# Optimization experiments

Hardware: AMD Instinct MI355X
Metric: run time of the kernel (lower is better)

## Reference

```python
import jax, jax.numpy as jnp
import numpy as np

B, N, D, L, H, DH, M, FF = 4, 2048, 512, 6, 8, 64, 266, 2048
EPS_LN = 1e-5
KERNEL_EPS = 1e-4


def fixed_pos_emb(n, dim):
    # performer_pytorch FixedPositionalEmbedding: cat(sin, cos) over half-dims
    inv_freq = 1.0 / (10000.0 ** (jnp.arange(0, dim, 2, dtype=jnp.float32) / dim))
    t = jnp.arange(n, dtype=jnp.float32)
    s = jnp.einsum('i,j->ij', t, inv_freq)  # [n, dim//2]
    return jnp.concatenate([jnp.sin(s), jnp.cos(s)], axis=-1)  # [n, dim]


def layer_norm(x, g, b):
    mu = x.mean(-1, keepdims=True)
    var = ((x - mu) ** 2).mean(-1, keepdims=True)
    return (x - mu) * jax.lax.rsqrt(var + EPS_LN) * g + b


def rotate_every_two(t):
    t1 = t[..., ::2]
    t2 = t[..., 1::2]
    return jnp.stack([-t2, t1], axis=-1).reshape(t.shape)


def apply_rotary(q, k, sinu):
    # sinu: [n, DH] = cat(sin_half, cos_half); repeat each value twice (interleaved)
    half = sinu.shape[-1] // 2
    sin = jnp.repeat(sinu[:, :half], 2, axis=-1)  # [n, DH]
    cos = jnp.repeat(sinu[:, half:], 2, axis=-1)
    q = q * cos + rotate_every_two(q) * sin
    k = k * cos + rotate_every_two(k) * sin
    return q, k


def softmax_kernel(data, proj, is_query):
    # data: [B,H,N,DH], proj: [M,DH]
    d = data.shape[-1]
    data_normalizer = d ** -0.25
    ratio = proj.shape[0] ** -0.5
    data_dash = jnp.einsum('bhnd,md->bhnm', data * data_normalizer, proj)
    diag = (data ** 2).sum(-1) * 0.5 * (data_normalizer ** 2)  # [B,H,N]
    if is_query:
        m = jnp.max(data_dash, axis=-1, keepdims=True)
    else:
        m = jnp.max(data_dash)
    return ratio * (jnp.exp(data_dash - diag[..., None] - m) + KERNEL_EPS)


def linear_attention(qf, kf, v):
    # qf/kf: [B,H,N,M], v: [B,H,N,DH]  (non-causal FAVOR+)
    k_sum = kf.sum(axis=-2)  # [B,H,M]
    d_inv = 1.0 / jnp.einsum('bhnm,bhm->bhn', qf, k_sum)
    context = jnp.einsum('bhnm,bhne->bhme', kf, v)  # [B,H,M,DH]
    return jnp.einsum('bhme,bhnm,bhn->bhne', context, qf, d_inv)


def setup_inputs() -> dict:
    key = jax.random.key(0)
    ks = jax.random.split(key, 8)
    std = 0.02
    inp = {
        'x': jax.random.normal(ks[0], (B, N, D), jnp.float32),
        'Wq': jax.random.normal(ks[1], (L, D, H * DH), jnp.float32) * std,
        'Wk': jax.random.normal(ks[2], (L, D, H * DH), jnp.float32) * std,
        'Wv': jax.random.normal(ks[3], (L, D, H * DH), jnp.float32) * std,
        'Wo': jax.random.normal(ks[4], (L, H * DH, D), jnp.float32) * std,
        'proj': jax.random.normal(ks[5], (L, M, DH), jnp.float32),
        'ln1_g': jnp.ones((L, D), jnp.float32),
        'ln1_b': jnp.zeros((L, D), jnp.float32),
        'W1': jax.random.normal(ks[6], (L, D, FF), jnp.float32) * std,
        'b1': jnp.zeros((L, FF), jnp.float32),
        'W2': jax.random.normal(ks[7], (L, FF, D), jnp.float32) * std,
        'b2': jnp.zeros((L, D), jnp.float32),
        'ln2_g': jnp.ones((L, D), jnp.float32),
        'ln2_b': jnp.zeros((L, D), jnp.float32),
        'lnf_g': jnp.ones((D,), jnp.float32),
        'lnf_b': jnp.zeros((D,), jnp.float32),
    }
    return inp


def reference(x, Wq, Wk, Wv, Wo, proj, ln1_g, ln1_b, W1, b1, W2, b2, ln2_g, ln2_b, lnf_g, lnf_b):
    n = x.shape[1]
    x = x + fixed_pos_emb(n, D)[None]          # additive sinusoidal emb
    sinu = fixed_pos_emb(n, DH)                 # per-head rotary table [n, DH]
    for i in range(L):
        # --- PreLayerNorm FAVOR+ self-attention ---
        h = layer_norm(x, ln1_g[i], ln1_b[i])
        q = jnp.einsum('bnd,de->bne', h, Wq[i]).reshape(B, n, H, DH).transpose(0, 2, 1, 3)
        k = jnp.einsum('bnd,de->bne', h, Wk[i]).reshape(B, n, H, DH).transpose(0, 2, 1, 3)
        v = jnp.einsum('bnd,de->bne', h, Wv[i]).reshape(B, n, H, DH).transpose(0, 2, 1, 3)
        q, k = apply_rotary(q, k, sinu)
        qf = softmax_kernel(q, proj[i], True)
        kf = softmax_kernel(k, proj[i], False)
        o = linear_attention(qf, kf, v)         # [B,H,n,DH]
        o = o.transpose(0, 2, 1, 3).reshape(B, n, H * DH)
        x = x + jnp.einsum('bne,ed->bnd', o, Wo[i])
        # --- PreLayerNorm FFN (GELU) ---
        h = layer_norm(x, ln2_g[i], ln2_b[i])
        h = jax.nn.gelu(jnp.einsum('bnd,df->bnf', h, W1[i]) + b1[i], approximate=False)
        x = x + jnp.einsum('bnf,fd->bnd', h, W2[i]) + b2[i]
    return layer_norm(x, lnf_g, lnf_b)
```

## Files before the change

kernel.cpp:

```cpp
#include <hip/hip_runtime.h>
#include <hip/hip_bf16.h>
#include <cstdint>

typedef float v4f __attribute__((ext_vector_type(4)));
typedef short v8s __attribute__((ext_vector_type(8)));
typedef unsigned short u16;

#define N_SEQ 2048
#define D_MODEL 512
#define N_LAYER 6
#define N_HEAD 8
#define D_HEAD 64
#define M_FEAT 266
#define M_PAD 288
#define M_ALLOC 384
#define FF_DIM 2048
#define BATCH 4
#define ROWS 8192
#define BHN 65536

__device__ __forceinline__ float b2f(u16 u) {
  return __uint_as_float(((uint32_t)u) << 16);
}
__device__ __forceinline__ u16 f2b(float f) {
  union { __hip_bfloat16 h; u16 u; } c;
  c.h = __float2bfloat16(f);
  return c.u;
}
__device__ __forceinline__ float wave_sum(float v) {
#pragma unroll
  for (int o = 1; o < 64; o <<= 1) v += __shfl_xor(v, o);
  return v;
}
__device__ __forceinline__ float wave_max(float v) {
#pragma unroll
  for (int o = 1; o < 64; o <<= 1) v = fmaxf(v, __shfl_xor(v, o));
  return v;
}

__device__ __forceinline__ float gelu_f(float x) {
  float ax = fabsf(x) * 0.70710678118f;
  float tt = __builtin_amdgcn_rcpf(fmaf(0.3275911f, ax, 1.0f));
  float poly = tt * fmaf(tt, fmaf(tt, fmaf(tt, fmaf(tt, 1.061405429f, -1.453152027f),
                                           1.421413741f), -0.284496736f), 0.254829592f);
  float er = 1.0f - poly * __expf(-ax * ax);
  er = copysignf(er, x);
  return 0.5f * x * (1.0f + er);
}

__device__ __forceinline__ void mfma_bf16(v4f& d, v8s a, v8s b) {
  asm volatile("v_mfma_f32_16x16x32_bf16 %0, %1, %2, %0" : "+v"(d) : "v"(a), "v"(b));
}

__device__ __forceinline__ void async16(const u16* g, u16* l) {
  __builtin_amdgcn_global_load_lds(
      (const __attribute__((address_space(1))) uint32_t*)g,
      (__attribute__((address_space(3))) uint32_t*)l, 16, 0, 0);
}

template <int EPI, int KSPLIT>
__global__ void __launch_bounds__(512, 4)
gemm3s(const u16* __restrict__ A, const u16* __restrict__ B,
       void* __restrict__ Cv, const float* __restrict__ bias,
       int K, int ldc)
{
  extern __shared__ u16 lds[];
  const int t = threadIdx.x;
  const int lane = t & 63;
  const int w = t >> 6;
  const int wm = w >> 2;
  const int wn = w & 3;
  const int tiM = blockIdx.x << 7, tiN = blockIdx.y << 8;
  const int ks = (KSPLIT > 1) ? blockIdx.z : 0;
  const int kchunk = K / KSPLIT;
  const int NT = kchunk >> 5;

  const int rr = lane & 15;
  const int kq = (lane >> 4) << 3;
  const int sw = ((rr >> 1) & 3) << 3;
  const int cr = kq ^ sw;

  const int srow = t >> 2;
  const int scol = (((t & 3) ^ ((srow >> 1) & 3)) << 3);
  const u16* Abase = A + (long long)(tiM + srow) * K + scol + (long long)ks * kchunk;
  const u16* Bbase = B + (long long)(tiN + srow) * K + scol + (long long)ks * kchunk;
  const long long r128 = 128LL * K;

  v4f acc[4][4] = {};

  auto stage3 = [&](int s, int kt) {
    const long long k0 = (long long)kt * 32;
    u16* d = &lds[s * 12288 + t * 8];
    async16(Abase + k0, d);
    async16(Bbase + k0, d + 4096);
    async16(Bbase + k0 + r128, d + 8192);
  };

  stage3(0, 0);
  stage3(1, 1);
  asm volatile("s_waitcnt vmcnt(3)" ::: "memory");
  __builtin_amdgcn_s_barrier();

  for (int kt = 0; kt < NT; ++kt) {
    const int s = kt % 3;
    const int sp = (kt + 2) % 3;
    const bool st = (kt + 2 < NT);
    const int ab = s * 12288;
    const int bb = ab + 4096;
    v8s af[4], bf[4];
#pragma unroll
    for (int i = 0; i < 4; i++) {
      af[i] = *(const v8s*)&lds[ab + (wm * 64 + i * 16 + rr) * 32 + cr];
      bf[i] = *(const v8s*)&lds[bb + (wn * 64 + i * 16 + rr) * 32 + cr];
    }
    if (st) stage3(sp, kt + 2);
    __builtin_amdgcn_s_setprio(1);
#pragma unroll
    for (int m = 0; m < 4; m++)
#pragma unroll
      for (int n = 0; n < 4; n++) mfma_bf16(acc[m][n], af[m], bf[n]);
    __builtin_amdgcn_s_setprio(0);
    if (st) asm volatile("s_waitcnt vmcnt(3)" ::: "memory");
    else    asm volatile("s_waitcnt vmcnt(0)" ::: "memory");
    __builtin_amdgcn_s_barrier();
  }

  __builtin_amdgcn_sched_barrier(0);
  asm volatile("s_nop 7\ns_nop 7\ns_nop 7");
  __builtin_amdgcn_sched_barrier(0);

  const int r4 = (lane >> 4) << 2;
  const int cc = lane & 15;
#pragma unroll
  for (int mf = 0; mf < 4; mf++)
#pragma unroll
    for (int nf = 0; nf < 4; nf++)
#pragma unroll
      for (int i = 0; i < 4; i++) {
        int row = tiM + wm * 64 + mf * 16 + r4 + i;
        int col = tiN + wn * 64 + nf * 16 + cc;
        float v = acc[mf][nf][i];
        if (EPI == 0) {
          ((u16*)Cv)[(long long)row * ldc + col] = f2b(v);
        } else if (EPI == 3) {
          ((u16*)Cv)[(long long)row * ldc + col] = f2b(gelu_f(v + bias[col]));
        } else {
          ((float*)Cv)[((long long)ks * ROWS + row) * ldc + col] = v;
        }
      }
}

__global__ void ff2red(const float* __restrict__ part, const float* __restrict__ bias,
                       float* __restrict__ x)
{
  long long i = ((long long)blockIdx.x * 256 + threadIdx.x) * 8;
  int col = (int)(i & 511);
  v4f s0 = {}, s1 = {};
#pragma unroll
  for (int ks = 0; ks < 4; ks++) {
    const float* p = part + (long long)ks * (ROWS * 512LL) + i;
    s0 += *(const v4f*)p;
    s1 += *(const v4f*)(p + 4);
  }
  v4f b0 = *(const v4f*)(bias + col);
  v4f b1 = *(const v4f*)(bias + col + 4);
  v4f x0 = *(const v4f*)(x + i), x1 = *(const v4f*)(x + i + 4);
  x0 += s0 + b0;
  x1 += s1 + b1;
  *(v4f*)(x + i) = x0;
  *(v4f*)(x + i + 4) = x1;
}

template <int EPI, int BN, int KSPLIT>
__global__ void __launch_bounds__(256, 4)
gemm2(const u16* __restrict__ A, const u16* __restrict__ B,
      void* __restrict__ Cv, const float* __restrict__ bias,
      int K, int ldc, long long sA, long long sB, long long sC,
      float scale, int Ncap, int Mcap, unsigned int* __restrict__ gmax)
{
  __shared__ u16 As[2][128 * 32];
  __shared__ u16 Bs[2][BN * 32];
  __shared__ float smax[4];
  const int zz = blockIdx.z;
  const int z = (KSPLIT > 1) ? zz / KSPLIT : zz;
  const int ks = (KSPLIT > 1) ? zz % KSPLIT : 0;
  const int kchunk = K / KSPLIT;
  const u16* Ag = A + (long long)z * sA + ks * kchunk;
  const u16* Bg = B + (long long)z * sB + ks * kchunk;
  const int t = threadIdx.x;
  const int lane = t & 63;
  const int w = t >> 6;
  constexpr int NF = BN / 32;
  const int wm = (w >> 1) << 6;
  const int wn = (w & 1) * (BN / 2);
  const int tiM = blockIdx.x << 7, tiN = blockIdx.y * BN;

  const int srow = t >> 2;
  const int scol = (t & 3) << 3;
  const u16* Ap = Ag + (long long)(tiM + srow) * K + scol;
  const u16* Bp = Bg + (long long)(tiN + srow) * K + scol;
  const long long rstride = 64LL * K;

  const int rr = lane & 15;
  const int kc = (lane >> 4) << 3;

  v4f acc[4][NF] = {};

  const int nk = kchunk >> 5;
  auto stage = [&](int buf, int k0) {
    async16(Ap + k0, &As[buf][t * 8]);
    async16(Ap + k0 + rstride, &As[buf][t * 8 + 2048]);
    async16(Bp + k0, &Bs[buf][t * 8]);
    if (BN == 128) async16(Bp + k0 + rstride, &Bs[buf][t * 8 + 2048]);
  };

  stage(0, 0);
  __syncthreads();
  int cur = 0;
  for (int kt = 0; kt < nk; ++kt) {
    if (kt + 1 < nk) stage(cur ^ 1, (kt + 1) << 5);
    v8s af[4], bf[NF];
#pragma unroll
    for (int i = 0; i < 4; i++) af[i] = *(const v8s*)&As[cur][(wm + rr + i * 16) * 32 + kc];
#pragma unroll
    for (int i = 0; i < NF; i++) bf[i] = *(const v8s*)&Bs[cur][(wn + rr + i * 16) * 32 + kc];
#pragma unroll
    for (int fm = 0; fm < 4; fm++)
#pragma unroll
      for (int fn = 0; fn < NF; fn++)
        mfma_bf16(acc[fm][fn], af[fm], bf[fn]);
    __syncthreads();
    cur ^= 1;
  }

  __builtin_amdgcn_sched_barrier(0);
  asm volatile("s_nop 7\ns_nop 7\ns_nop 7");
  __builtin_amdgcn_sched_barrier(0);

  const int r4 = (lane >> 4) << 2;
  const int cc = lane & 15;
  float lmax = -3e38f;
#pragma unroll
  for (int fm = 0; fm < 4; fm++)
#pragma unroll
    for (int fn = 0; fn < NF; fn++)
#pragma unroll
      for (int i = 0; i < 4; i++) {
        int row = tiM + wm + fm * 16 + r4 + i;
        int col = tiN + wn + fn * 16 + cc;
        float v = acc[fm][fn][i];
        if (EPI == 5) {
          if (row < Mcap && col < Ncap)
            ((float*)Cv)[((long long)zz * M_ALLOC + row) * 64 + col] = v;
        } else if (EPI == 7) {
          if (col < M_FEAT) lmax = fmaxf(lmax, v * scale);
        }
      }

  if (EPI == 7) {
    lmax = wave_max(lmax);
    if (lane == 0) smax[w] = lmax;
    __syncthreads();
    if (t == 0) {
      float m = fmaxf(fmaxf(smax[0], smax[1]), fmaxf(smax[2], smax[3]));
      unsigned int u = __float_as_uint(m);
      unsigned int key = (u & 0x80000000u) ? ~u : (u | 0x80000000u);
      atomicMax(gmax, key);
    }
  }
}

__global__ void __launch_bounds__(384, 3)
kf_gemm(const u16* __restrict__ kr, const u16* __restrict__ proj,
        const float* __restrict__ diagk, const unsigned int* __restrict__ kmax,
        u16* __restrict__ kfT, float* __restrict__ part)
{
  __shared__ u16 As[2][288 * 32];
  __shared__ u16 Bs[2][64 * 32];
  __shared__ float sdg[64];
  const int ntile = blockIdx.x;
  const int bh = blockIdx.z;
  const int n0 = ntile << 6;
  const int t = threadIdx.x;
  const int lane = t & 63;
  const int w = t >> 6;
  const u16* Bg = kr + (long long)bh * (N_SEQ * 64) + (long long)n0 * 64;
  const int rr = lane & 15, kc = (lane >> 4) << 3;

  if (t < 64) sdg[t] = diagk[(long long)bh * N_SEQ + n0 + t];
  unsigned int kk = kmax[0];
  const float km = (kk & 0x80000000u) ? __uint_as_float(kk ^ 0x80000000u)
                                      : __uint_as_float(~kk);

  v4f acc[3][4] = {};
  auto stage = [&](int buf, int k0) {
#pragma unroll
    for (int j = 0; j < 3; j++) {
      int idx = j * 384 + t;
      async16(proj + (long long)(idx >> 2) * 64 + ((idx & 3) << 3) + k0,
              &As[buf][j * 3072 + t * 8]);
    }
    if (t < 256) async16(Bg + (long long)(t >> 2) * 64 + ((t & 3) << 3) + k0,
                         &Bs[buf][t * 8]);
  };

  stage(0, 0);
  __syncthreads();
  for (int kt = 0; kt < 2; ++kt) {
    if (kt == 0) stage(1, 32);
    v8s af[3], bf[4];
#pragma unroll
    for (int i = 0; i < 3; i++) af[i] = *(const v8s*)&As[kt][(w * 48 + i * 16 + rr) * 32 + kc];
#pragma unroll
    for (int i = 0; i < 4; i++) bf[i] = *(const v8s*)&Bs[kt][(i * 16 + rr) * 32 + kc];
#pragma unroll
    for (int fm = 0; fm < 3; fm++)
#pragma unroll
      for (int fn = 0; fn < 4; fn++)
        mfma_bf16(acc[fm][fn], af[fm], bf[fn]);
    __syncthreads();
  }

  __builtin_amdgcn_sched_barrier(0);
  asm volatile("s_nop 7\ns_nop 7\ns_nop 7");
  __builtin_amdgcn_sched_barrier(0);

  const int r4 = (lane >> 4) << 2;
  const int cc = lane & 15;
  const float sc = 0.35355339f;

#pragma unroll
  for (int fm = 0; fm < 3; fm++)
#pragma unroll
    for (int i = 0; i < 4; i++) {
      int m = w * 48 + fm * 16 + r4 + i;
      float s = 0.0f;
#pragma unroll
      for (int fn = 0; fn < 4; fn++) {
        float dd = acc[fm][fn][i] * sc;
        float kf = (m < M_FEAT)
            ? 0.06131389f * (__expf(dd - sdg[fn * 16 + cc] - km) + 1e-4f) : 0.0f;
        acc[fm][fn][i] = kf;
        s += kf;
        kfT[((long long)bh * M_ALLOC + m) * N_SEQ + n0 + fn * 16 + cc] = f2b(kf);
      }
#pragma unroll
      for (int o = 1; o < 16; o <<= 1) s += __shfl_xor(s, o);
      if (cc == 0) part[((long long)bh * M_PAD + m) * 32 + ntile] = s;
    }
}

__global__ void ksumred(const float* __restrict__ part, float* __restrict__ ksum)
{
  int i = blockIdx.x * 256 + threadIdx.x;
  if (i >= 32 * M_PAD) return;
  const float* p = part + (long long)i * 32;
  float s = 0.0f;
#pragma unroll
  for (int j = 0; j < 32; j += 4) {
    v4f v = *(const v4f*)(p + j);
    s += v[0] + v[1] + v[2] + v[3];
  }
  ksum[i] = s;
}

template <int EPI>
__global__ void __launch_bounds__(256, 6)
gemm_small(const u16* __restrict__ A, const u16* __restrict__ B,
           void* __restrict__ Cv, const float* __restrict__ bias,
           int K, int ldc, long long sA, long long sB)
{
  __shared__ u16 As[2][64 * 32];
  __shared__ u16 Bs[2][64 * 32];
  const int z = blockIdx.z;
  const u16* Ag = A + (long long)z * sA;
  const u16* Bg = B + (long long)z * sB;
  const int t = threadIdx.x;
  const int lane = t & 63;
  const int w = t >> 6;
  const int wm = (w >> 1) << 5;
  const int wn = (w & 1) << 5;
  const int tiM = blockIdx.x << 6, tiN = blockIdx.y << 6;

  const int srow = t >> 2;
  const int scol = (t & 3) << 3;
  const u16* Ap = Ag + (long long)(tiM + srow) * K + scol;
  const u16* Bp = Bg + (long long)(tiN + srow) * K + scol;

  const int rr = lane & 15;
  const int kc = (lane >> 4) << 3;

  v4f acc[2][2] = {};

  const int nk = K >> 5;
  auto stage = [&](int buf, int k0) {
    async16(Ap + k0, &As[buf][t * 8]);
    async16(Bp + k0, &Bs[buf][t * 8]);
  };

  stage(0, 0);
  __syncthreads();
  int cur = 0;
  for (int kt = 0; kt < nk; ++kt) {
    if (kt + 1 < nk) stage(cur ^ 1, (kt + 1) << 5);
    v8s af[2], bf[2];
#pragma unroll
    for (int i = 0; i < 2; i++) af[i] = *(const v8s*)&As[cur][(wm + rr + i * 16) * 32 + kc];
#pragma unroll
    for (int i = 0; i < 2; i++) bf[i] = *(const v8s*)&Bs[cur][(wn + rr + i * 16) * 32 + kc];
#pragma unroll
    for (int fm = 0; fm < 2; fm++)
#pragma unroll
      for (int fn = 0; fn < 2; fn++)
        mfma_bf16(acc[fm][fn], af[fm], bf[fn]);
    __syncthreads();
    cur ^= 1;
  }

  __builtin_amdgcn_sched_barrier(0);
  asm volatile("s_nop 7\ns_nop 7\ns_nop 7");
  __builtin_amdgcn_sched_barrier(0);

  const int r4 = (lane >> 4) << 2;
  const int cc = lane & 15;
#pragma unroll
  for (int fm = 0; fm < 2; fm++)
#pragma unroll
    for (int fn = 0; fn < 2; fn++)
#pragma unroll
      for (int i = 0; i < 4; i++) {
        int row = tiM + wm + fm * 16 + r4 + i;
        int col = tiN + wn + fn * 16 + cc;
        float v = acc[fm][fn][i];
        if (EPI == 2) {
          long long idx = (long long)row * ldc + col;
          float bb = bias ? bias[col] : 0.0f;
          ((float*)Cv)[idx] += v + bb;
        } else {
          int b_ = z >> 3, h_ = z & 7;
          ((u16*)Cv)[(long long)(b_ * N_SEQ + row) * 512 + h_ * 64 + col] = f2b(v);
        }
      }
}

__global__ void __launch_bounds__(384, 3)
ddq_qf(const u16* __restrict__ qr, const u16* __restrict__ proj,
       const float* __restrict__ diag, const float* __restrict__ ksum,
       u16* __restrict__ qf)
{
  __shared__ u16 As[2][64 * 32];
  __shared__ u16 Bs[2][288 * 32];
  __shared__ float redw[6][64];
  __shared__ float rowv[64];
  __shared__ float sdg[64];
  const int bh = blockIdx.z;
  const int tiM = blockIdx.x << 6;
  const int t = threadIdx.x;
  const int lane = t & 63;
  const int w = t >> 6;
  const u16* Ag = qr + (long long)bh * (N_SEQ * 64);
  const int srow = t >> 2, scol = (t & 3) << 3;
  const u16* Ap = Ag + (long long)(tiM + srow) * 64 + scol;
  const int rr = lane & 15, kc = (lane >> 4) << 3;
  const int wn = w * 48;

  if (t < 64) sdg[t] = diag[(long long)bh * N_SEQ + tiM + t];

  v4f acc[4][3] = {};
  auto stage = [&](int buf, int k0) {
    if (t < 256) async16(Ap + k0, &As[buf][t * 8]);
#pragma unroll
    for (int j = 0; j < 3; j++) {
      int idx = j * 384 + t;
      async16(proj + (long long)(idx >> 2) * 64 + ((idx & 3) << 3) + k0,
              &Bs[buf][j * 3072 + t * 8]);
    }
  };

  stage(0, 0);
  __syncthreads();
  for (int kt = 0; kt < 2; ++kt) {
    if (kt == 0) stage(1, 32);
    v8s af[4], bf[3];
#pragma unroll
    for (int i = 0; i < 4; i++) af[i] = *(const v8s*)&As[kt][(rr + i * 16) * 32 + kc];
#pragma unroll
    for (int i = 0; i < 3; i++) bf[i] = *(const v8s*)&Bs[kt][(wn + i * 16 + rr) * 32 + kc];
#pragma unroll
    for (int fm = 0; fm < 4; fm++)
#pragma unroll
      for (int fn = 0; fn < 3; fn++)
        mfma_bf16(acc[fm][fn], af[fm], bf[fn]);
    __syncthreads();
  }

  __builtin_amdgcn_sched_barrier(0);
  asm volatile("s_nop 7\ns_nop 7\ns_nop 7");
  __builtin_amdgcn_sched_barrier(0);

  const int r4 = (lane >> 4) << 2;
  const int cc = lane & 15;
  const float sc = 0.35355339f;

#pragma unroll
  for (int fm = 0; fm < 4; fm++)
#pragma unroll
    for (int i = 0; i < 4; i++) {
      float m = -3e38f;
#pragma unroll
      for (int fn = 0; fn < 3; fn++) {
        int col = wn + fn * 16 + cc;
        float v = acc[fm][fn][i] * sc;
        if (col < M_FEAT) m = fmaxf(m, v);
      }
#pragma unroll
      for (int o = 1; o < 16; o <<= 1) m = fmaxf(m, __shfl_xor(m, o));
      if (cc == 0) redw[w][fm * 16 + r4 + i] = m;
    }
  __syncthreads();
  if (t < 64) {
    float g = redw[0][t];
#pragma unroll
    for (int ww = 1; ww < 6; ww++) g = fmaxf(g, redw[ww][t]);
    rowv[t] = g;
  }
  __syncthreads();

  float ksv[3];
#pragma unroll
  for (int fn = 0; fn < 3; fn++) ksv[fn] = ksum[bh * M_PAD + wn + fn * 16 + cc];

#pragma unroll
  for (int fm = 0; fm < 4; fm++)
#pragma unroll
    for (int i = 0; i < 4; i++) {
      int row = fm * 16 + r4 + i;
      float gm = rowv[row];
      float dg = sdg[row];
      float s = 0.0f;
#pragma unroll
      for (int fn = 0; fn < 3; fn++) {
        float e = 0.06131389f * (__expf(acc[fm][fn][i] * sc - dg - gm) + 1e-4f);
        acc[fm][fn][i] = e;
        s += e * ksv[fn];
      }
#pragma unroll
      for (int o = 1; o < 16; o <<= 1) s += __shfl_xor(s, o);
      if (cc == 0) redw[w][row] = s;
    }
  __syncthreads();
  if (t < 64) {
    float s = redw[0][t];
#pragma unroll
    for (int ww = 1; ww < 6; ww++) s += redw[ww][t];
    rowv[t] = 1.0f / s;
  }
  __syncthreads();

#pragma unroll
  for (int fm = 0; fm < 4; fm++)
#pragma unroll
    for (int i = 0; i < 4; i++) {
      int row = fm * 16 + r4 + i;
      float dinv = rowv[row];
#pragma unroll
      for (int fn = 0; fn < 3; fn++) {
        int col = wn + fn * 16 + cc;
        qf[((long long)bh * N_SEQ + tiM + row) * M_PAD + col] =
            f2b(acc[fm][fn][i] * dinv);
      }
    }
}

template <bool F32OUT>
__global__ void ln_kernel(const float* __restrict__ x, const float* __restrict__ g,
                          const float* __restrict__ b, void* __restrict__ out)
{
  const int row = blockIdx.x * 4 + (threadIdx.x >> 6);
  const int lane = threadIdx.x & 63;
  const float* xr = x + (long long)row * D_MODEL + lane * 8;
  v4f v0 = *(const v4f*)xr;
  v4f v1 = *(const v4f*)(xr + 4);
  float s = v0[0] + v0[1] + v0[2] + v0[3] + v1[0] + v1[1] + v1[2] + v1[3];
  float sq = v0[0]*v0[0] + v0[1]*v0[1] + v0[2]*v0[2] + v0[3]*v0[3]
           + v1[0]*v1[0] + v1[1]*v1[1] + v1[2]*v1[2] + v1[3]*v1[3];
  s = wave_sum(s);
  sq = wave_sum(sq);
  float mu = s * (1.0f / D_MODEL);
  float var = sq * (1.0f / D_MODEL) - mu * mu;
  float rstd = rsqrtf(var + 1e-5f);
  v4f g0 = *(const v4f*)(g + lane * 8), g1 = *(const v4f*)(g + lane * 8 + 4);
  v4f bb0 = *(const v4f*)(b + lane * 8), bb1 = *(const v4f*)(b + lane * 8 + 4);
  float y[8];
#pragma unroll
  for (int j = 0; j < 4; j++) y[j] = (v0[j] - mu) * rstd * g0[j] + bb0[j];
#pragma unroll
  for (int j = 0; j < 4; j++) y[4 + j] = (v1[j] - mu) * rstd * g1[j] + bb1[j];
  if (F32OUT) {
    float* op = (float*)out + (long long)row * D_MODEL + lane * 8;
    v4f o0 = {y[0], y[1], y[2], y[3]}, o1 = {y[4], y[5], y[6], y[7]};
    *(v4f*)op = o0;
    *(v4f*)(op + 4) = o1;
  } else {
    u16* op = (u16*)out + (long long)row * D_MODEL + lane * 8;
    alignas(16) u16 tmp[8];
#pragma unroll
    for (int j = 0; j < 8; j++) tmp[j] = f2b(y[j]);
    *(v8s*)op = *(v8s*)tmp;
  }
}

__global__ void posadd(const float* __restrict__ xin, float* __restrict__ x)
{
  long long i = (long long)blockIdx.x * 256 + threadIdx.x;
  int d = (int)(i & 511);
  int n = (int)((i >> 9) & 2047);
  int j = d & 255;
  float sarg = (float)n * expf(-0.035977892f * (float)j);
  float pe = (d < 256) ? sinf(sarg) : cosf(sarg);
  x[i] = xin[i] + pe;
}

__global__ void rotab(float* __restrict__ ts, float* __restrict__ tc)
{
  int i = blockIdx.x * 64 + threadIdx.x;
  int n = i >> 5, j = i & 31;
  float sarg = (float)n * expf(-0.28782314f * (float)j);
  float s, c;
  sincosf(sarg, &s, &c);
  ts[i] = s;
  tc[i] = c;
}

__global__ void rotary_kernel(const u16* __restrict__ qkv,
                              const float* __restrict__ ts, const float* __restrict__ tc,
                              u16* __restrict__ qr, u16* __restrict__ kr,
                              float* __restrict__ dq, float* __restrict__ dk)
{
  int bid = blockIdx.x * 4 + (threadIdx.x >> 6);
  int n = bid & 2047;
  int h = (bid >> 11) & 7;
  int b = bid >> 14;
  int lane = threadIdx.x & 63;
  long long src = ((long long)(b * N_SEQ + n)) * 1536 + h * 64 + lane;
  float qv = b2f(qkv[src]);
  float kv = b2f(qkv[src + 512]);
  int j = lane >> 1;
  float sn = ts[n * 32 + j], cn = tc[n * 32 + j];
  float qp = __shfl_xor(qv, 1), kp = __shfl_xor(kv, 1);
  float qrv = (lane & 1) ? (qv * cn + qp * sn) : (qv * cn - qp * sn);
  float krv = (lane & 1) ? (kv * cn + kp * sn) : (kv * cn - kp * sn);
  u16 qb = f2b(qrv), kb = f2b(krv);
  long long dst = ((long long)bid) * 64 + lane;
  qr[dst] = qb;
  kr[dst] = kb;
  float q2 = b2f(qb); q2 *= q2;
  float k2 = b2f(kb); k2 *= k2;
  q2 = wave_sum(q2);
  k2 = wave_sum(k2);
  if (lane == 0) { dq[bid] = q2 * 0.0625f; dk[bid] = k2 * 0.0625f; }
}

__global__ void vtrans(const u16* __restrict__ qkv, u16* __restrict__ vT)
{
  int bid = blockIdx.x;
  int nt = bid & 31;
  int h = (bid >> 5) & 7;
  int b = bid >> 8;
  __shared__ u16 st[64][72];
  int t = threadIdx.x;
  int r = t >> 2, c = (t & 3) << 4;
  long long src = ((long long)(b * N_SEQ + nt * 64 + r)) * 1536 + 1024 + h * 64 + c;
  *(v8s*)&st[r][c] = *(const v8s*)(qkv + src);
  *(v8s*)&st[r][c + 8] = *(const v8s*)(qkv + src + 8);
  __syncthreads();
  alignas(16) u16 tmp[16];
#pragma unroll
  for (int jj = 0; jj < 16; jj++) tmp[jj] = st[c + jj][r];
  long long dst = ((long long)((b * 8 + h) * 64 + r)) * N_SEQ + nt * 64 + c;
  *(v8s*)(vT + dst) = *(v8s*)&tmp[0];
  *(v8s*)(vT + dst + 8) = *(v8s*)&tmp[8];
}

__global__ void wtrans(const float* __restrict__ src, u16* __restrict__ dst,
                       int Ks, int Ns, long long sSrc, long long sDst)
{
  int l = blockIdx.z;
  src += (long long)l * sSrc;
  dst += (long long)l * sDst;
  int n0 = blockIdx.x << 6, k0 = blockIdx.y << 6;
  __shared__ float st[64][68];
  int t = threadIdx.x;
  int r = t >> 2, c = (t & 3) << 4;
  const float* sp = src + (long long)(k0 + r) * Ns + n0 + c;
#pragma unroll
  for (int jj = 0; jj < 16; jj += 4) *(v4f*)&st[r][c + jj] = *(const v4f*)(sp + jj);
  __syncthreads();
  alignas(16) u16 tmp[16];
#pragma unroll
  for (int jj = 0; jj < 16; jj++) tmp[jj] = f2b(st[c + jj][r]);
  u16* dp = dst + (long long)(n0 + r) * Ks + k0 + c;
  *(v8s*)(dp) = *(v8s*)&tmp[0];
  *(v8s*)(dp + 8) = *(v8s*)&tmp[8];
}

__global__ void projconv(const float* __restrict__ proj, u16* __restrict__ out)
{
  int i = blockIdx.x * 256 + threadIdx.x;
  int dh = i & 63;
  int m = (i >> 6) % M_ALLOC;
  int l = i / (M_ALLOC * 64);
  float v = (m < M_FEAT) ? proj[((long long)l * M_FEAT + m) * 64 + dh] : 0.0f;
  out[i] = f2b(v);
}

__global__ void resetmax(unsigned int* p) { *p = 0u; }

__global__ void ctxred(const float* __restrict__ part, u16* __restrict__ ctxT)
{
  int bh = blockIdx.y;
  int m0 = blockIdx.x << 6;
  __shared__ float st[64][65];
  int t = threadIdx.x;
  int r = t >> 2, c = (t & 3) << 4;
  int m = m0 + r;
  v4f s[4] = {};
  if (m < M_PAD) {
    for (int ks = 0; ks < 8; ks++) {
      const float* p = part + (((long long)bh * 8 + ks) * M_ALLOC + m) * 64 + c;
#pragma unroll
      for (int j = 0; j < 4; j++) s[j] += *(const v4f*)(p + j * 4);
    }
  }
#pragma unroll
  for (int j = 0; j < 4; j++)
#pragma unroll
    for (int e = 0; e < 4; e++) st[r][c + j * 4 + e] = s[j][e];
  __syncthreads();
  int e = t >> 2, mc = (t & 3) << 4;
  if (m0 + mc < M_PAD) {
    alignas(16) u16 tmp[16];
#pragma unroll
    for (int j = 0; j < 16; j++) tmp[j] = f2b(st[mc + j][e]);
    u16* op = ctxT + ((long long)bh * 64 + e) * M_PAD + m0 + mc;
    *(v8s*)op = *(v8s*)&tmp[0];
    *(v8s*)(op + 8) = *(v8s*)&tmp[8];
  }
}

extern "C" void kernel_launch(void* const* d_in, const int* in_sizes, int n_in,
                              void* d_out, int out_size, void* d_ws, size_t ws_size,
                              hipStream_t stream)
{
  const float* x_in = (const float*)d_in[0];
  const float* Wq  = (const float*)d_in[1];
  const float* Wk  = (const float*)d_in[2];
  const float* Wv  = (const float*)d_in[3];
  const float* Wo  = (const float*)d_in[4];
  const float* Pr  = (const float*)d_in[5];
  const float* ln1g = (const float*)d_in[6];
  const float* ln1b = (const float*)d_in[7];
  const float* W1  = (const float*)d_in[8];
  const float* b1  = (const float*)d_in[9];
  const float* W2  = (const float*)d_in[10];
  const float* b2  = (const float*)d_in[11];
  const float* ln2g = (const float*)d_in[12];
  const float* ln2b = (const float*)d_in[13];
  const float* lnfg = (const float*)d_in[14];
  const float* lnfb = (const float*)d_in[15];

  hipFuncSetAttribute(reinterpret_cast<const void*>(&gemm3s<0, 1>),
                      hipFuncAttributeMaxDynamicSharedMemorySize, 73728);
  hipFuncSetAttribute(reinterpret_cast<const void*>(&gemm3s<3, 1>),
                      hipFuncAttributeMaxDynamicSharedMemorySize, 73728);
  hipFuncSetAttribute(reinterpret_cast<const void*>(&gemm3s<5, 4>),
                      hipFuncAttributeMaxDynamicSharedMemorySize, 73728);

  char* ws = (char*)d_ws;
  size_t off = 0;
  auto alloc = [&](size_t bytes) -> void* {
    void* p = ws + off;
    off = (off + bytes + 255) & ~(size_t)255;
    return p;
  };

  float* x      = (float*)alloc((size_t)ROWS * D_MODEL * 4);
  float* tsin   = (float*)alloc((size_t)N_SEQ * 32 * 4);
  float* tcos   = (float*)alloc((size_t)N_SEQ * 32 * 4);
  u16*   wqkvT  = (u16*)alloc((size_t)N_LAYER * 1536 * 512 * 2);
  u16*   woT    = (u16*)alloc((size_t)N_LAYER * 512 * 512 * 2);
  u16*   w1T    = (u16*)alloc((size_t)N_LAYER * 2048 * 512 * 2);
  u16*   w2T    = (u16*)alloc((size_t)N_LAYER * 512 * 2048 * 2);
  u16*   projT  = (u16*)alloc((size_t)N_LAYER * M_ALLOC * 64 * 2);
  u16*   hbuf   = (u16*)alloc((size_t)ROWS * D_MODEL * 2);
  u16*   obuf   = (u16*)alloc((size_t)ROWS * D_MODEL * 2);
  float* big    = (float*)alloc((size_t)32 * N_SEQ * M_PAD * 4);
  u16*   qrbuf  = (u16*)alloc((size_t)BHN * 64 * 2);
  u16*   krbuf  = (u16*)alloc((size_t)BHN * 64 * 2);
  u16*   vTbuf  = (u16*)alloc((size_t)BHN * 64 * 2);
  float* diagq  = (float*)alloc((size_t)BHN * 4);
  float* diagk  = (float*)alloc((size_t)BHN * 4);
  unsigned int* kmaxu = (unsigned int*)alloc(256);
  u16*   kfT    = (u16*)alloc((size_t)32 * M_ALLOC * N_SEQ * 2);
  float* part   = (float*)alloc((size_t)32 * 8 * M_ALLOC * 64 * 4);
  float* kspart = (float*)alloc((size_t)32 * M_PAD * 32 * 4);
  u16*   ctxT   = (u16*)alloc((size_t)32 * 64 * M_PAD * 2);
  float* ksum   = (float*)alloc((size_t)32 * M_PAD * 4);
  (void)alloc(1 << 20);
  (void)ws_size; (void)in_sizes; (void)n_in; (void)out_size;
  float* ff2part = (float*)kfT;

  posadd<<<16384, 256, 0, stream>>>(x_in, x);
  rotab<<<1024, 64, 0, stream>>>(tsin, tcos);
  wtrans<<<dim3(8, 8, 6), 256, 0, stream>>>(Wq, wqkvT, 512, 512, 512LL * 512, 1536LL * 512);
  wtrans<<<dim3(8, 8, 6), 256, 0, stream>>>(Wk, wqkvT + 512LL * 512, 512, 512, 512LL * 512, 1536LL * 512);
  wtrans<<<dim3(8, 8, 6), 256, 0, stream>>>(Wv, wqkvT + 1024LL * 512, 512, 512, 512LL * 512, 1536LL * 512);
  wtrans<<<dim3(8, 8, 6), 256, 0, stream>>>(Wo, woT, 512, 512, 512LL * 512, 512LL * 512);
  wtrans<<<dim3(32, 8, 6), 256, 0, stream>>>(W1, w1T, 512, 2048, 512LL * 2048, 2048LL * 512);
  wtrans<<<dim3(8, 32, 6), 256, 0, stream>>>(W2, w2T, 2048, 512, 2048LL * 512, 512LL * 2048);
  projconv<<<(N_LAYER * M_ALLOC * 64) / 256, 256, 0, stream>>>(Pr, projT);

  for (int l = 0; l < N_LAYER; l++) {
    const u16* wq = wqkvT + (long long)l * 1536 * 512;
    const u16* wo = woT + (long long)l * 512 * 512;
    const u16* w1 = w1T + (long long)l * 2048 * 512;
    const u16* w2 = w2T + (long long)l * 512 * 2048;
    const u16* pj = projT + (long long)l * M_ALLOC * 64;

    resetmax<<<1, 1, 0, stream>>>(kmaxu);
    ln_kernel<false><<<ROWS / 4, 256, 0, stream>>>(x, ln1g + l * 512, ln1b + l * 512, hbuf);
    gemm3s<0, 1><<<dim3(64, 6), 512, 73728, stream>>>(hbuf, wq, big, nullptr, 512, 1536);
    rotary_kernel<<<BHN / 4, 256, 0, stream>>>((u16*)big, tsin, tcos, qrbuf, krbuf, diagq, diagk);
    vtrans<<<1024, 256, 0, stream>>>((u16*)big, vTbuf);
    gemm2<7, 128, 1><<<dim3(512, 3, 1), 256, 0, stream>>>(krbuf, pj, nullptr, nullptr,
        64, M_PAD, 0, 0, 0, 0.35355339f, M_PAD, BHN, kmaxu);
    kf_gemm<<<dim3(32, 1, 32), 384, 0, stream>>>(krbuf, pj, diagk, kmaxu, kfT, kspart);
    ksumred<<<(32 * M_PAD + 255) / 256, 256, 0, stream>>>(kspart, ksum);
    gemm2<5, 64, 8><<<dim3(3, 1, 256), 256, 0, stream>>>(kfT, vTbuf, part, nullptr,
        2048, 64, (long long)M_ALLOC * N_SEQ, 64LL * N_SEQ, 0, 1.0f, 64, M_PAD, nullptr);
    ctxred<<<dim3(5, 32), 256, 0, stream>>>(part, ctxT);
    ddq_qf<<<dim3(32, 1, 32), 384, 0, stream>>>(qrbuf, pj, diagq, ksum, kfT);
    gemm_small<4><<<dim3(32, 1, 32), 256, 0, stream>>>(kfT, ctxT, obuf, nullptr,
        M_PAD, 0, (long long)N_SEQ * M_PAD, 64LL * M_PAD);
    gemm_small<2><<<dim3(128, 8, 1), 256, 0, stream>>>(obuf, wo, x, nullptr,
        512, 512, 0, 0);
    ln_kernel<false><<<ROWS / 4, 256, 0, stream>>>(x, ln2g + l * 512, ln2b + l * 512, hbuf);
    gemm3s<3, 1><<<dim3(64, 8), 512, 73728, stream>>>(hbuf, w1, big, b1 + (long long)l * 2048,
        512, 2048);
    gemm3s<5, 4><<<dim3(64, 2, 4), 512, 73728, stream>>>((u16*)big, w2, ff2part, nullptr,
        2048, 512);
    ff2red<<<2048, 256, 0, stream>>>(ff2part, b2 + (long long)l * 512, x);
  }

  ln_kernel<true><<<ROWS / 4, 256, 0, stream>>>(x, lnfg, lnfb, d_out);
}
```

Before: 1.474 ms.

## Fuse FF2 reduction with next LayerNorm and merge rotary with V transpose

The split-K FF2 reduction kernel now also computes the following layer's LN1, or the final LayerNorm on the last layer, so one launch and a re-read of x per layer go away. The rotary and V-transpose kernels become one kernel that reads q, k and v with vectorized 16-byte loads. The diag sums now use the fp32 rotated values instead of the bf16-rounded ones, and LN variance uses E[x^2]-mu^2, both with small numeric differences. In the 3-stage GEMM loop, the next async stage is issued before the LDS fragment reads.

```diff
diff --git a/kernel.cpp b/kernel.cpp
--- a/kernel.cpp
+++ b/kernel.cpp
@@ -107,13 +107,13 @@
     const bool st = (kt + 2 < NT);
     const int ab = s * 12288;
     const int bb = ab + 4096;
+    if (st) stage3(sp, kt + 2);
     v8s af[4], bf[4];
 #pragma unroll
     for (int i = 0; i < 4; i++) {
       af[i] = *(const v8s*)&lds[ab + (wm * 64 + i * 16 + rr) * 32 + cr];
       bf[i] = *(const v8s*)&lds[bb + (wn * 64 + i * 16 + rr) * 32 + cr];
     }
-    if (st) stage3(sp, kt + 2);
     __builtin_amdgcn_s_setprio(1);
 #pragma unroll
     for (int m = 0; m < 4; m++)
@@ -150,25 +150,56 @@
       }
 }
 
-__global__ void ff2red(const float* __restrict__ part, const float* __restrict__ bias,
-                       float* __restrict__ x)
-{
-  long long i = ((long long)blockIdx.x * 256 + threadIdx.x) * 8;
-  int col = (int)(i & 511);
+template <bool LAST>
+__global__ void ff2red_ln(const float* __restrict__ part, const float* __restrict__ bias,
+                          float* __restrict__ x, const float* __restrict__ g,
+                          const float* __restrict__ bvec, void* __restrict__ out)
+{
+  const int row = blockIdx.x * 4 + (threadIdx.x >> 6);
+  const int lane = threadIdx.x & 63;
+  const long long base = (long long)row * D_MODEL + lane * 8;
   v4f s0 = {}, s1 = {};
 #pragma unroll
   for (int ks = 0; ks < 4; ks++) {
-    const float* p = part + (long long)ks * (ROWS * 512LL) + i;
+    const float* p = part + (long long)ks * (ROWS * 512LL) + base;
     s0 += *(const v4f*)p;
     s1 += *(const v4f*)(p + 4);
   }
-  v4f b0 = *(const v4f*)(bias + col);
-  v4f b1 = *(const v4f*)(bias + col + 4);
-  v4f x0 = *(const v4f*)(x + i), x1 = *(const v4f*)(x + i + 4);
-  x0 += s0 + b0;
-  x1 += s1 + b1;
-  *(v4f*)(x + i) = x0;
-  *(v4f*)(x + i + 4) = x1;
+  v4f b0 = *(const v4f*)(bias + lane * 8);
+  v4f b1 = *(const v4f*)(bias + lane * 8 + 4);
+  v4f x0 = *(const v4f*)(x + base) + s0 + b0;
+  v4f x1 = *(const v4f*)(x + base + 4) + s1 + b1;
+  if (!LAST) {
+    *(v4f*)(x + base) = x0;
+    *(v4f*)(x + base + 4) = x1;
+  }
+  float s = x0[0] + x0[1] + x0[2] + x0[3] + x1[0] + x1[1] + x1[2] + x1[3];
+  float sq = x0[0]*x0[0] + x0[1]*x0[1] + x0[2]*x0[2] + x0[3]*x0[3]
+           + x1[0]*x1[0] + x1[1]*x1[1] + x1[2]*x1[2] + x1[3]*x1[3];
+  s = wave_sum(s);
+  sq = wave_sum(sq);
+  float mu = s * (1.0f / D_MODEL);
+  float var = sq * (1.0f / D_MODEL) - mu * mu;
+  float rstd = rsqrtf(var + 1e-5f);
+  v4f g0 = *(const v4f*)(g + lane * 8), g1 = *(const v4f*)(g + lane * 8 + 4);
+  v4f bb0 = *(const v4f*)(bvec + lane * 8), bb1 = *(const v4f*)(bvec + lane * 8 + 4);
+  float y[8];
+#pragma unroll
+  for (int j = 0; j < 4; j++) y[j] = (x0[j] - mu) * rstd * g0[j] + bb0[j];
+#pragma unroll
+  for (int j = 0; j < 4; j++) y[4 + j] = (x1[j] - mu) * rstd * g1[j] + bb1[j];
+  if (LAST) {
+    float* op = (float*)out + base;
+    v4f o0 = {y[0], y[1], y[2], y[3]}, o1 = {y[4], y[5], y[6], y[7]};
+    *(v4f*)op = o0;
+    *(v4f*)(op + 4) = o1;
+  } else {
+    u16* op = (u16*)out + base;
+    alignas(16) u16 tmp[8];
+#pragma unroll
+    for (int j = 0; j < 8; j++) tmp[j] = f2b(y[j]);
+    *(v8s*)op = *(v8s*)tmp;
+  }
 }
 
 template <int EPI, int BN, int KSPLIT>
@@ -632,52 +663,61 @@
   tc[i] = c;
 }
 
-__global__ void rotary_kernel(const u16* __restrict__ qkv,
-                              const float* __restrict__ ts, const float* __restrict__ tc,
-                              u16* __restrict__ qr, u16* __restrict__ kr,
-                              float* __restrict__ dq, float* __restrict__ dk)
-{
-  int bid = blockIdx.x * 4 + (threadIdx.x >> 6);
-  int n = bid & 2047;
-  int h = (bid >> 11) & 7;
-  int b = bid >> 14;
-  int lane = threadIdx.x & 63;
-  long long src = ((long long)(b * N_SEQ + n)) * 1536 + h * 64 + lane;
-  float qv = b2f(qkv[src]);
-  float kv = b2f(qkv[src + 512]);
-  int j = lane >> 1;
-  float sn = ts[n * 32 + j], cn = tc[n * 32 + j];
-  float qp = __shfl_xor(qv, 1), kp = __shfl_xor(kv, 1);
-  float qrv = (lane & 1) ? (qv * cn + qp * sn) : (qv * cn - qp * sn);
-  float krv = (lane & 1) ? (kv * cn + kp * sn) : (kv * cn - kp * sn);
-  u16 qb = f2b(qrv), kb = f2b(krv);
-  long long dst = ((long long)bid) * 64 + lane;
-  qr[dst] = qb;
-  kr[dst] = kb;
-  float q2 = b2f(qb); q2 *= q2;
-  float k2 = b2f(kb); k2 *= k2;
-  q2 = wave_sum(q2);
-  k2 = wave_sum(k2);
-  if (lane == 0) { dq[bid] = q2 * 0.0625f; dk[bid] = k2 * 0.0625f; }
-}
-
-__global__ void vtrans(const u16* __restrict__ qkv, u16* __restrict__ vT)
-{
-  int bid = blockIdx.x;
-  int nt = bid & 31;
-  int h = (bid >> 5) & 7;
-  int b = bid >> 8;
+__global__ void __launch_bounds__(256)
+rotvt(const u16* __restrict__ qkv,
+      const float* __restrict__ ts, const float* __restrict__ tc,
+      u16* __restrict__ qr, u16* __restrict__ kr, u16* __restrict__ vT,
+      float* __restrict__ dq, float* __restrict__ dk)
+{
   __shared__ u16 st[64][72];
-  int t = threadIdx.x;
-  int r = t >> 2, c = (t & 3) << 4;
-  long long src = ((long long)(b * N_SEQ + nt * 64 + r)) * 1536 + 1024 + h * 64 + c;
-  *(v8s*)&st[r][c] = *(const v8s*)(qkv + src);
-  *(v8s*)&st[r][c + 8] = *(const v8s*)(qkv + src + 8);
-  __syncthreads();
+  const int bid = blockIdx.x;
+  const int nt = bid & 31;
+  const int h = (bid >> 5) & 7;
+  const int b = bid >> 8;
+  const int t = threadIdx.x;
+  const int r = t >> 3;
+  const int cg = t & 7;
+#pragma unroll
+  for (int it = 0; it < 2; ++it) {
+    const int nl = it * 32 + r;
+    const int n = nt * 64 + nl;
+    const long long src = ((long long)(b * N_SEQ + n)) * 1536 + h * 64 + cg * 8;
+    v8s q8 = *(const v8s*)(qkv + src);
+    v8s k8 = *(const v8s*)(qkv + src + 512);
+    v8s v8 = *(const v8s*)(qkv + src + 1024);
+    v4f sn = *(const v4f*)(ts + n * 32 + cg * 4);
+    v4f cn = *(const v4f*)(tc + n * 32 + cg * 4);
+    alignas(16) u16 qo[8], ko[8];
+    float q2 = 0.0f, k2 = 0.0f;
+#pragma unroll
+    for (int j = 0; j < 4; j++) {
+      float qe = b2f((u16)q8[2 * j]), qoe = b2f((u16)q8[2 * j + 1]);
+      float ke = b2f((u16)k8[2 * j]), koe = b2f((u16)k8[2 * j + 1]);
+      float c = cn[j], s = sn[j];
+      float q0 = qe * c - qoe * s, q1 = qoe * c + qe * s;
+      float k0 = ke * c - koe * s, k1 = koe * c + ke * s;
+      qo[2 * j] = f2b(q0); qo[2 * j + 1] = f2b(q1);
+      ko[2 * j] = f2b(k0); ko[2 * j + 1] = f2b(k1);
+      q2 += q0 * q0 + q1 * q1;
+      k2 += k0 * k0 + k1 * k1;
+    }
+    q2 += __shfl_xor(q2, 1); q2 += __shfl_xor(q2, 2); q2 += __shfl_xor(q2, 4);
+    k2 += __shfl_xor(k2, 1); k2 += __shfl_xor(k2, 2); k2 += __shfl_xor(k2, 4);
+    const long long rowidx = (long long)(b * 8 + h) * N_SEQ + n;
+    if (cg == 0) {
+      dq[rowidx] = q2 * 0.0625f;
+      dk[rowidx] = k2 * 0.0625f;
+    }
+    *(v8s*)(qr + rowidx * 64 + cg * 8) = *(v8s*)qo;
+    *(v8s*)(kr + rowidx * 64 + cg * 8) = *(v8s*)ko;
+    *(v8s*)&st[nl][cg * 8] = v8;
+  }
+  __syncthreads();
+  const int r2 = t >> 2, c2 = (t & 3) << 4;
   alignas(16) u16 tmp[16];
 #pragma unroll
-  for (int jj = 0; jj < 16; jj++) tmp[jj] = st[c + jj][r];
-  long long dst = ((long long)((b * 8 + h) * 64 + r)) * N_SEQ + nt * 64 + c;
+  for (int jj = 0; jj < 16; jj++) tmp[jj] = st[c2 + jj][r2];
+  const long long dst = ((long long)((b * 8 + h) * 64 + r2)) * N_SEQ + nt * 64 + c2;
   *(v8s*)(vT + dst) = *(v8s*)&tmp[0];
   *(v8s*)(vT + dst + 8) = *(v8s*)&tmp[8];
 }
@@ -820,6 +860,8 @@
   wtrans<<<dim3(8, 32, 6), 256, 0, stream>>>(W2, w2T, 2048, 512, 2048LL * 512, 512LL * 2048);
   projconv<<<(N_LAYER * M_ALLOC * 64) / 256, 256, 0, stream>>>(Pr, projT);
 
+  ln_kernel<false><<<ROWS / 4, 256, 0, stream>>>(x, ln1g, ln1b, hbuf);
+
   for (int l = 0; l < N_LAYER; l++) {
     const u16* wq = wqkvT + (long long)l * 1536 * 512;
     const u16* wo = woT + (long long)l * 512 * 512;
@@ -828,10 +870,8 @@
     const u16* pj = projT + (long long)l * M_ALLOC * 64;
 
     resetmax<<<1, 1, 0, stream>>>(kmaxu);
-    ln_kernel<false><<<ROWS / 4, 256, 0, stream>>>(x, ln1g + l * 512, ln1b + l * 512, hbuf);
     gemm3s<0, 1><<<dim3(64, 6), 512, 73728, stream>>>(hbuf, wq, big, nullptr, 512, 1536);
-    rotary_kernel<<<BHN / 4, 256, 0, stream>>>((u16*)big, tsin, tcos, qrbuf, krbuf, diagq, diagk);
-    vtrans<<<1024, 256, 0, stream>>>((u16*)big, vTbuf);
+    rotvt<<<1024, 256, 0, stream>>>((u16*)big, tsin, tcos, qrbuf, krbuf, vTbuf, diagq, diagk);
     gemm2<7, 128, 1><<<dim3(512, 3, 1), 256, 0, stream>>>(krbuf, pj, nullptr, nullptr,
         64, M_PAD, 0, 0, 0, 0.35355339f, M_PAD, BHN, kmaxu);
     kf_gemm<<<dim3(32, 1, 32), 384, 0, stream>>>(krbuf, pj, diagk, kmaxu, kfT, kspart);
@@ -849,8 +889,12 @@
         512, 2048);
     gemm3s<5, 4><<<dim3(64, 2, 4), 512, 73728, stream>>>((u16*)big, w2, ff2part, nullptr,
         2048, 512);
-    ff2red<<<2048, 256, 0, stream>>>(ff2part, b2 + (long long)l * 512, x);
-  }
-
-  ln_kernel<true><<<ROWS / 4, 256, 0, stream>>>(x, lnfg, lnfb, d_out);
-}
+    if (l < N_LAYER - 1) {
+      ff2red_ln<false><<<2048, 256, 0, stream>>>(ff2part, b2 + (long long)l * 512, x,
+          ln1g + (long long)(l + 1) * 512, ln1b + (long long)(l + 1) * 512, hbuf);
+    } else {
+      ff2red_ln<true><<<2048, 256, 0, stream>>>(ff2part, b2 + (long long)l * 512, x,
+          lnfg, lnfb, d_out);
+    }
+  }
+}
```

Result: faster. 1.409 ms (-4.5%).
